# Optimization experiments

Measured on AMD Instinct MI355X. Metric: run time of the kernel, lower is better.

Reference implementation:

```python
import jax, jax.numpy as jnp
import numpy as np

B, S, D, H = 4, 4096, 512, 8


def setup_inputs() -> dict:
    key = jax.random.key(0)
    ks = jax.random.split(key, 9)
    s = 1.0 / np.sqrt(D)
    return {
        "x": jax.random.normal(ks[0], (B, S, D), jnp.float32),
        "Wq": jax.random.normal(ks[1], (D, D), jnp.float32) * s,
        "bq": jax.random.normal(ks[2], (D,), jnp.float32) * 0.02,
        "Wk": jax.random.normal(ks[3], (D, D), jnp.float32) * s,
        "bk": jax.random.normal(ks[4], (D,), jnp.float32) * 0.02,
        "Wv": jax.random.normal(ks[5], (D, D), jnp.float32) * s,
        "bv": jax.random.normal(ks[6], (D,), jnp.float32) * 0.02,
        "Wo": jax.random.normal(ks[7], (H * D, D), jnp.float32) * (1.0 / np.sqrt(H * D)),
        "bo": jax.random.normal(ks[8], (D,), jnp.float32) * 0.02,
        "num_heads": H,
    }


def reference(x, Wq, bq, Wk, bk, Wv, bv, Wo, bo, num_heads):
    # Q/K/V projections (self-attention path; encoder_output=None)
    q = x @ Wq + bq  # [B,S,D]
    k = x @ Wk + bk
    v = x @ Wv + bv
    scale = 1.0 / jnp.sqrt(jnp.asarray(x.shape[-1], x.dtype))
    scores = jnp.einsum("bqd,bkd->bqk", q, k) * scale  # [B,S,S]
    probs = jax.nn.softmax(scores, axis=-1)
    attn = jnp.einsum("bqk,bkd->bqd", probs, v)  # [B,S,D]
    # Original stacks identical heads then torch.cat along dim=-1 -> tile H copies.
    cat = jnp.tile(attn, (1, 1, num_heads))  # [B,S,H*D]
    return cat @ Wo + bo  # [B,S,D]
```

## Files before the change

kernel.cpp:

```cpp
#include <hip/hip_runtime.h>
#include <stdint.h>

#define SCALE 0.04419417382415922f

typedef __bf16 bf16x8 __attribute__((ext_vector_type(8)));
typedef float f32x4 __attribute__((ext_vector_type(4)));
typedef uint16_t u16x8 __attribute__((ext_vector_type(8)));

static __device__ __forceinline__ uint16_t f2bf(float f) {
  union { float f; uint32_t u; } v; v.f = f;
  uint32_t u = v.u;
  return (uint16_t)((u + 0x7FFFu + ((u >> 16) & 1u)) >> 16);
}
static __device__ __forceinline__ float bf2f(uint16_t h) {
  union { uint32_t u; float f; } v; v.u = ((uint32_t)h) << 16;
  return v.f;
}

static __device__ __forceinline__ void gload16(const void* g, void* l) {
  __builtin_amdgcn_global_load_lds(
      (__attribute__((address_space(1))) void*)g,
      (__attribute__((address_space(3))) void*)l, 16, 0, 0);
}

#define P_BAR asm volatile("s_barrier" ::: "memory")
#define P_LGKM do { asm volatile("s_waitcnt lgkmcnt(0)" ::: "memory"); \
                    __builtin_amdgcn_sched_barrier(0); } while (0)


__global__ __launch_bounds__(256)
void convert_x(const float* __restrict__ x, uint16_t* __restrict__ xb) {
  size_t i = ((size_t)blockIdx.x * 256 + threadIdx.x) * 8;
  float4 a = *(const float4*)(x + i);
  float4 b = *(const float4*)(x + i + 4);
  u16x8 o;
  o[0] = f2bf(a.x); o[1] = f2bf(a.y); o[2] = f2bf(a.z); o[3] = f2bf(a.w);
  o[4] = f2bf(b.x); o[5] = f2bf(b.y); o[6] = f2bf(b.z); o[7] = f2bf(b.w);
  *(u16x8*)(xb + i) = o;
}

__global__ __launch_bounds__(256)
void pack_wraw(const float* __restrict__ Wq, const float* __restrict__ Wk,
               uint16_t* __restrict__ oq, uint16_t* __restrict__ ok) {
  size_t i = ((size_t)blockIdx.x * 256 + threadIdx.x) * 8;
  const float* src = blockIdx.y ? Wk : Wq;
  uint16_t* dst = blockIdx.y ? ok : oq;
  const float scl = blockIdx.y ? 1.0f : SCALE;
  float4 a = *(const float4*)(src + i);
  float4 b = *(const float4*)(src + i + 4);
  u16x8 o;
  o[0] = f2bf(a.x * scl); o[1] = f2bf(a.y * scl);
  o[2] = f2bf(a.z * scl); o[3] = f2bf(a.w * scl);
  o[4] = f2bf(b.x * scl); o[5] = f2bf(b.y * scl);
  o[6] = f2bf(b.z * scl); o[7] = f2bf(b.w * scl);
  *(u16x8*)(dst + i) = o;
}

__global__ __launch_bounds__(256)
void pack_wv(const float* __restrict__ Wv, uint16_t* __restrict__ wvT) {
  __shared__ float tile[64][65];
  const int k0 = blockIdx.x * 64, n0 = blockIdx.y * 64;
  const int t = threadIdx.x, r = t >> 2, c0 = (t & 3) * 16;
  #pragma unroll
  for (int j = 0; j < 4; j++) {
    float4 v = *(const float4*)&Wv[(size_t)(k0 + r) * 512 + n0 + c0 + j * 4];
    tile[r][c0 + j * 4 + 0] = v.x; tile[r][c0 + j * 4 + 1] = v.y;
    tile[r][c0 + j * 4 + 2] = v.z; tile[r][c0 + j * 4 + 3] = v.w;
  }
  __syncthreads();
  u16x8 o0, o1;
  #pragma unroll
  for (int e = 0; e < 8; e++) {
    o0[e] = f2bf(tile[c0 + e][r]);
    o1[e] = f2bf(tile[c0 + 8 + e][r]);
  }
  uint16_t* dst = wvT + (size_t)(n0 + r) * 512 + k0 + c0;
  *(u16x8*)dst = o0;
  *(u16x8*)(dst + 8) = o1;
}

__global__ __launch_bounds__(256)
void pack_wo(const float* __restrict__ Wo, uint16_t* __restrict__ woT) {
  __shared__ float tile[64][65];
  const int k0 = blockIdx.x * 64, n0 = blockIdx.y * 64;
  const int t = threadIdx.x, r = t >> 2, c0 = (t & 3) * 16;
  float av[16];
  #pragma unroll
  for (int e = 0; e < 16; e++) av[e] = 0.f;
  for (int h = 0; h < 8; h++) {
    const float* src = &Wo[(size_t)(h * 512 + k0 + r) * 512 + n0 + c0];
    #pragma unroll
    for (int j = 0; j < 4; j++) {
      float4 v = *(const float4*)(src + j * 4);
      av[j * 4 + 0] += v.x; av[j * 4 + 1] += v.y;
      av[j * 4 + 2] += v.z; av[j * 4 + 3] += v.w;
    }
  }
  #pragma unroll
  for (int e = 0; e < 16; e++) tile[r][c0 + e] = av[e];
  __syncthreads();
  u16x8 o0, o1;
  #pragma unroll
  for (int e = 0; e < 8; e++) {
    o0[e] = f2bf(tile[c0 + e][r]);
    o1[e] = f2bf(tile[c0 + 8 + e][r]);
  }
  uint16_t* dst = woT + (size_t)(n0 + r) * 512 + k0 + c0;
  *(u16x8*)dst = o0;
  *(u16x8*)(dst + 8) = o1;
}

__global__ void pack_byv(const float* __restrict__ bv, float* __restrict__ byv) {
  int i = blockIdx.x * 256 + threadIdx.x;
  if (i < 512) byv[i] = 0.f;
  else if (i < 1024) byv[i] = bv[i - 512];
}

__global__ __launch_bounds__(512)
void pack_gc(const float* __restrict__ Wk, const float* __restrict__ bq,
             const float* __restrict__ bk, float* __restrict__ g) {
  __shared__ float red[512];
  const int m = threadIdx.x;
  float s = 0.f;
  for (int d = 0; d < 512; ++d) s += Wk[(size_t)m * 512 + d] * bq[d];
  g[m] = s * SCALE;
  red[m] = bk[m] * bq[m];
  __syncthreads();
  for (int o = 256; o; o >>= 1) {
    if (m < o) red[m] += red[m + o];
    __syncthreads();
  }
  if (m == 0) g[512] = red[0] * SCALE;
}

__global__ __launch_bounds__(256)
void c_vec(const uint16_t* __restrict__ xb, const float* __restrict__ g,
           float* __restrict__ cv) {
  __shared__ float gs[513];
  const int t = threadIdx.x;
  for (int i = t; i < 513; i += 256) gs[i] = g[i];
  __syncthreads();
  const int r = blockIdx.x * 32 + (t >> 3);
  const int j = t & 7;
  const uint16_t* p = xb + (size_t)r * 512 + j * 64;
  float s = 0.f;
  #pragma unroll
  for (int q = 0; q < 8; q++) {
    u16x8 v = *(const u16x8*)(p + q * 8);
    #pragma unroll
    for (int e = 0; e < 8; e++) s += bf2f(v[e]) * gs[j * 64 + q * 8 + e];
  }
  s += __shfl_xor(s, 1); s += __shfl_xor(s, 2); s += __shfl_xor(s, 4);
  if (j == 0) cv[r] = s + gs[512];
}

__global__ __launch_bounds__(256)
void transpose_v(const uint16_t* __restrict__ yv, uint16_t* __restrict__ Vt) {
  __shared__ uint16_t tile[64][72];
  const int s0 = blockIdx.x * 64, d0 = blockIdx.y * 64, b = blockIdx.z;
  const int t = threadIdx.x, r = t >> 2, c0 = (t & 3) * 16;
  const uint16_t* src = yv + ((size_t)(b * 4096 + s0 + r)) * 1024 + 512 + d0 + c0;
  *(u16x8*)&tile[r][c0] = *(const u16x8*)src;
  *(u16x8*)&tile[r][c0 + 8] = *(const u16x8*)(src + 8);
  __syncthreads();
  u16x8 o0, o1;
  #pragma unroll
  for (int e = 0; e < 8; e++) { o0[e] = tile[c0 + e][r]; o1[e] = tile[c0 + 8 + e][r]; }
  uint16_t* dst = Vt + ((size_t)b * 512 + d0 + r) * 4096 + s0 + c0;
  *(u16x8*)dst = o0;
  *(u16x8*)(dst + 8) = o1;
}

template<int BN, int MODE>
static __device__ __forceinline__
void gemm8_body(const uint16_t* __restrict__ A, const uint16_t* __restrict__ Bt,
                const float* __restrict__ bias, void* __restrict__ Cout,
                const float* __restrict__ sums,
                int M, int N, int K, int lda, int ldb, int ldc,
                long long aZ, long long bZ, long long cZ, long long sZ,
                long long biasZ) {
  constexpr int NREP = BN / 64;
  constexpr int NH = NREP / 2;
  constexpr int WN = BN / 4;
  constexpr int BELTS = BN * 64;
  __shared__ uint16_t SH[32768 + 2 * BELTS];

  const int nbn = N / BN;
  const int nwg = (M >> 8) * nbn;
  int id = blockIdx.x;
  id = (id & 7) * (nwg >> 3) + (id >> 3);
  const int bm = id / nbn, bn = id % nbn;
  const long long z = blockIdx.z;
  A += z * aZ; Bt += z * bZ;
  const size_t m0 = (size_t)bm * 256, n0 = (size_t)bn * BN;

  const int t = threadIdx.x;
  const int lane = t & 63, w = t >> 6;
  const int wr = w >> 2, wc = w & 3;
  const int l15 = lane & 15, l4 = lane >> 4, l7 = lane & 7, l3 = lane >> 3;
  const int sw = l7 ^ l3;

  const uint16_t* srcA = A + (m0 + w * 8 + l3) * (size_t)lda + sw * 8;
  const uint16_t* srcB = (BN == 256)
      ? Bt + (n0 + (w >> 1) * 64 + (w & 1) * 16 + l3) * (size_t)ldb + sw * 8
      : Bt + (n0 + (w >> 1) * 32 + (w & 1) * 8 + l3) * (size_t)ldb + sw * 8;

  const int NKT = K >> 6;
  const int NIT = NKT >> 1;

  f32x4 acc[8][NREP];
  #pragma unroll
  for (int i = 0; i < 8; i++)
    #pragma unroll
    for (int j = 0; j < NREP; j++) acc[i][j] = (f32x4)(0.f);

  bf16x8 a[4][2], b0[NH][2], b1[NH][2];

  auto stageA = [&](int tile, int mh) {
    const uint16_t* s = srcA + mh * 64 * (size_t)lda + tile * 64;
    uint16_t* d = SH + (tile & 1) * 16384 + mh * 4096 + w * 512;
    gload16(s, d);
    gload16(s + 128 * (size_t)lda, d + 8192);
  };
  auto stageB = [&](int tile, int nh) {
    if (BN == 256) {
      const uint16_t* s = srcB + nh * 32 * (size_t)ldb + tile * 64;
      uint16_t* d = SH + 32768 + (tile & 1) * BELTS + (w >> 1) * 4096 + nh * 2048 + (w & 1) * 1024;
      gload16(s, d);
      gload16(s + 8 * (size_t)ldb, d + 512);
    } else {
      const uint16_t* s = srcB + nh * 16 * (size_t)ldb + tile * 64;
      uint16_t* d = SH + 32768 + (tile & 1) * BELTS + (w >> 1) * 2048 + nh * 1024 + (w & 1) * 512;
      gload16(s, d);
    }
  };
  auto loadA = [&](int buf, int mh) {
    const uint16_t* base = SH + buf * 16384 + (wr * 128 + mh * 64 + l15) * 64;
    #pragma unroll
    for (int m = 0; m < 4; m++)
      #pragma unroll
      for (int ks = 0; ks < 2; ks++)
        a[m][ks] = *(const bf16x8*)(base + m * 1024 + (((ks * 4 + l4) ^ l7) * 8));
  };
  auto loadB = [&](int buf, int nh, bf16x8 (&bd)[NH][2]) {
    const uint16_t* base = SH + 32768 + buf * BELTS + (wc * WN + nh * (WN / 2) + l15) * 64;
    #pragma unroll
    for (int n = 0; n < NH; n++)
      #pragma unroll
      for (int ks = 0; ks < 2; ks++)
        bd[n][ks] = *(const bf16x8*)(base + n * 1024 + (((ks * 4 + l4) ^ l7) * 8));
  };
  auto quad = [&](int mh, int nq, bf16x8 (&bq)[NH][2]) {
    __builtin_amdgcn_s_setprio(1);
    #pragma unroll
    for (int m = 0; m < 4; m++)
      #pragma unroll
      for (int n = 0; n < NH; n++)
        #pragma unroll
        for (int ks = 0; ks < 2; ks++)
          acc[mh * 4 + m][nq + n] = __builtin_amdgcn_mfma_f32_16x16x32_bf16(
              a[m][ks], bq[n][ks], acc[mh * 4 + m][nq + n], 0, 0, 0);
    __builtin_amdgcn_s_setprio(0);
  };

  stageA(0, 0); stageB(0, 0); stageA(0, 1); stageB(0, 1);
  stageA(1, 0); stageB(1, 0); stageA(1, 1);
  if (BN == 256) asm volatile("s_waitcnt vmcnt(6)" ::: "memory");
  else           asm volatile("s_waitcnt vmcnt(5)" ::: "memory");
  P_BAR;

  for (int k = 0; k < NIT - 1; ++k) {
    const int tt = 2 * k;
    loadA(0, 0); loadB(0, 0, b0); stageB(tt + 1, 1);
    P_BAR; P_LGKM; quad(0, 0, b0); P_BAR;
    loadB(0, 1, b1); stageA(tt + 2, 0);
    P_BAR; P_LGKM; quad(0, NH, b1); P_BAR;
    loadA(0, 1); stageB(tt + 2, 0);
    P_BAR; P_LGKM; quad(1, NH, b1); P_BAR;
    stageA(tt + 2, 1);
    if (BN == 256) asm volatile("s_waitcnt vmcnt(6)" ::: "memory");
    else           asm volatile("s_waitcnt vmcnt(5)" ::: "memory");
    P_BAR; quad(1, 0, b0); P_BAR;
    loadA(1, 0); loadB(1, 0, b0); stageB(tt + 2, 1);
    P_BAR; P_LGKM; quad(0, 0, b0); P_BAR;
    loadB(1, 1, b1); stageA(tt + 3, 0);
    P_BAR; P_LGKM; quad(0, NH, b1); P_BAR;
    loadA(1, 1); stageB(tt + 3, 0);
    P_BAR; P_LGKM; quad(1, NH, b1); P_BAR;
    stageA(tt + 3, 1);
    if (BN == 256) asm volatile("s_waitcnt vmcnt(6)" ::: "memory");
    else           asm volatile("s_waitcnt vmcnt(5)" ::: "memory");
    P_BAR; quad(1, 0, b0); P_BAR;
  }
  loadA(0, 0); loadB(0, 0, b0); stageB(NKT - 1, 1);
  P_BAR; P_LGKM; quad(0, 0, b0); P_BAR;
  loadB(0, 1, b1);
  P_BAR; P_LGKM; quad(0, NH, b1); P_BAR;
  loadA(0, 1);
  P_BAR; P_LGKM; quad(1, NH, b1); P_BAR;
  asm volatile("s_waitcnt vmcnt(0)" ::: "memory");
  P_BAR; quad(1, 0, b0); P_BAR;
  loadA(1, 0); loadB(1, 0, b0);
  P_BAR; P_LGKM; quad(0, 0, b0); P_BAR;
  loadB(1, 1, b1);
  P_BAR; P_LGKM; quad(0, NH, b1); P_BAR;
  loadA(1, 1);
  P_BAR; P_LGKM; quad(1, NH, b1); P_BAR;
  quad(1, 0, b0);

  asm volatile("s_waitcnt vmcnt(0) lgkmcnt(0)" ::: "memory");
  __syncthreads();

  const int g = l4;

  if (MODE == 1) {
    float bvv[NREP];
    #pragma unroll
    for (int ni = 0; ni < NREP; ni++) bvv[ni] = bias[n0 + wc * WN + ni * 16 + l15];
    float* C = (float*)Cout + z * cZ;
    #pragma unroll
    for (int am = 0; am < 8; am++)
      #pragma unroll
      for (int r = 0; r < 4; r++) {
        size_t gr = m0 + wr * 128 + am * 16 + g * 4 + r;
        #pragma unroll
        for (int ni = 0; ni < NREP; ni++)
          C[gr * (size_t)ldc + n0 + wc * WN + ni * 16 + l15] = acc[am][ni][r] + bvv[ni];
      }
    return;
  }

  if (MODE == 2) {
    float cvv[NREP];
    #pragma unroll
    for (int ni = 0; ni < NREP; ni++)
      cvv[ni] = bias[z * biasZ + n0 + wc * WN + ni * 16 + l15];
    float* sm = (float*)Cout;
    (void)sm;
    #pragma unroll
    for (int am = 0; am < 8; am++)
      #pragma unroll
      for (int r = 0; r < 4; r++) {
        float s = 0.f;
        #pragma unroll
        for (int ni = 0; ni < NREP; ni++) {
          float v = __expf(acc[am][ni][r] + cvv[ni]);
          acc[am][ni][r] = v;
          s += v;
        }
        s += __shfl_xor(s, 1); s += __shfl_xor(s, 2);
        s += __shfl_xor(s, 4); s += __shfl_xor(s, 8);
        if (l15 == 0)
          ((float*)sums)[z * sZ + (m0 + wr * 128 + am * 16 + g * 4 + r) * 64 +
                         (n0 >> 6) + wc] = s;
      }
  }

  float bvv[NREP];
  #pragma unroll
  for (int ni = 0; ni < NREP; ni++)
    bvv[ni] = (MODE == 0 && bias) ? bias[n0 + wc * WN + ni * 16 + l15] : 0.f;
  float4 sc[8];
  if (MODE == 3) {
    #pragma unroll
    for (int am = 0; am < 8; am++)
      sc[am] = *(const float4*)&sums[z * sZ + m0 + wr * 128 + am * 16 + g * 4];
  }

  constexpr int STR = BN + 8;
  uint16_t* C16 = (uint16_t*)Cout + z * cZ;
  #pragma unroll
  for (int h = 0; h < 2; ++h) {
    __syncthreads();
    if (wr == h) {
      #pragma unroll
      for (int am = 0; am < 8; am++)
        #pragma unroll
        for (int r = 0; r < 4; r++) {
          const int lr = am * 16 + g * 4 + r;
          #pragma unroll
          for (int ni = 0; ni < NREP; ni++) {
            float v = acc[am][ni][r] + bvv[ni];
            if (MODE == 3) v *= ((const float*)&sc[am])[r];
            SH[lr * STR + wc * WN + ni * 16 + l15] = f2bf(v);
          }
        }
    }
    __syncthreads();
    constexpr int CPT = BN / 32;
    #pragma unroll
    for (int c = 0; c < CPT; ++c) {
      const int idx = t + c * 512;
      const int row = idx / (BN / 8), c8 = idx % (BN / 8);
      *(u16x8*)(C16 + (m0 + h * 128 + row) * (size_t)ldc + n0 + c8 * 8) =
          *(const u16x8*)(SH + row * STR + c8 * 8);
    }
  }
}

__global__ __launch_bounds__(512, 2)
void w2_gemm(const uint16_t* A, const uint16_t* Bt, void* C) {
  gemm8_body<128, 0>(A, Bt, nullptr, C, nullptr, 512, 512, 512, 512, 512, 512,
                     0, 0, 0, 0, 0);
}
__global__ __launch_bounds__(512, 2)
void yv_gemm(const uint16_t* A, const uint16_t* Bt, const float* bias, void* C) {
  gemm8_body<256, 0>(A, Bt, bias, C, nullptr, 16384, 1024, 512, 512, 512, 1024,
                     0, 0, 0, 0, 0);
}
__global__ __launch_bounds__(512, 2)
void scores_gemm(const uint16_t* Y, const uint16_t* X, const float* cvec,
                 void* S, float* sums) {
  gemm8_body<256, 2>(Y, X, cvec, S, sums, 4096, 4096, 512, 1024, 512, 4096,
                     (long long)4096 * 1024, (long long)4096 * 512,
                     (long long)4096 * 4096, (long long)4096 * 64, 4096);
}
__global__ __launch_bounds__(512, 2)
void pv_gemm(const uint16_t* A, const uint16_t* Bt, void* C, const float* inv) {
  gemm8_body<128, 3>(A, Bt, nullptr, C, inv, 4096, 512, 4096, 4096, 4096, 512,
                     (long long)4096 * 4096, (long long)512 * 4096,
                     (long long)4096 * 512, 4096, 0);
}
__global__ __launch_bounds__(512, 2)
void out_gemm(const uint16_t* A, const uint16_t* Bt, const float* bias, void* C) {
  gemm8_body<128, 1>(A, Bt, bias, C, nullptr, 16384, 512, 512, 512, 512, 512,
                     0, 0, 0, 0, 0);
}

__global__ __launch_bounds__(256)
void reduce_sums(const float* __restrict__ P, float* __restrict__ inv, int rows) {
  int r = blockIdx.x * 256 + threadIdx.x;
  if (r >= rows) return;
  const float4* p4 = (const float4*)(P + (size_t)r * 64);
  float s = 0.f;
  #pragma unroll
  for (int i = 0; i < 16; ++i) { float4 v = p4[i]; s += (v.x + v.y) + (v.z + v.w); }
  inv[r] = 1.f / s;
}


extern "C" void kernel_launch(void* const* d_in, const int* in_sizes, int n_in,
                              void* d_out, int out_size, void* d_ws, size_t ws_size,
                              hipStream_t stream) {
  const float* x   = (const float*)d_in[0];
  const float* Wq  = (const float*)d_in[1];
  const float* bq  = (const float*)d_in[2];
  const float* Wk  = (const float*)d_in[3];
  const float* bk  = (const float*)d_in[4];
  const float* Wv  = (const float*)d_in[5];
  const float* bvp = (const float*)d_in[6];
  const float* Wo  = (const float*)d_in[7];
  const float* bo  = (const float*)d_in[8];
  float* out = (float*)d_out;

  char* ws = (char*)d_ws;
  const size_t MB = (size_t)1 << 20;
  uint16_t* xb   = (uint16_t*)(ws);
  uint16_t* yv   = (uint16_t*)(ws + 16 * MB);
  uint16_t* Vt   = (uint16_t*)(ws + 48 * MB);
  uint16_t* attn = (uint16_t*)(ws + 64 * MB);
  uint16_t* wqs  = (uint16_t*)(ws + 80 * MB);
  uint16_t* wkr  = (uint16_t*)(ws + 80 * MB + 512 * 1024);
  uint16_t* w2T  = (uint16_t*)(ws + 81 * MB);
  uint16_t* wvT  = (uint16_t*)(ws + 81 * MB + 512 * 1024);
  uint16_t* woT  = (uint16_t*)(ws + 82 * MB);
  float*    byv  = (float*)   (ws + 82 * MB + 512 * 1024);
  float*    g    = (float*)   (ws + 83 * MB);
  float*    sums = (float*)   (ws + 84 * MB);
  float*    invs = (float*)   (ws + 88 * MB);
  float*    cv   = (float*)   (ws + 89 * MB);
  uint16_t* Sbuf = (uint16_t*)(ws + 96 * MB);

  const int nz = (ws_size >= 225 * MB) ? 4 : 2;

  convert_x<<<dim3(4096), dim3(256), 0, stream>>>(x, xb);
  pack_wraw<<<dim3(128, 2), dim3(256), 0, stream>>>(Wq, Wk, wqs, wkr);
  pack_wv<<<dim3(8, 8), dim3(256), 0, stream>>>(Wv, wvT);
  pack_wo<<<dim3(8, 8), dim3(256), 0, stream>>>(Wo, woT);
  pack_byv<<<dim3(4), dim3(256), 0, stream>>>(bvp, byv);
  pack_gc<<<dim3(1), dim3(512), 0, stream>>>(Wk, bq, bk, g);

  w2_gemm<<<dim3(8, 1, 1), dim3(512), 0, stream>>>(wkr, wqs, w2T);

  yv_gemm<<<dim3(256, 1, 1), dim3(512), 0, stream>>>(xb, w2T, byv, yv);

  transpose_v<<<dim3(64, 8, 4), dim3(256), 0, stream>>>(yv, Vt);
  c_vec<<<dim3(512), dim3(256), 0, stream>>>(xb, g, cv);

  for (int p = 0; p < 4 / nz; ++p) {
    const uint16_t* Yp = yv + (size_t)p * nz * 4096 * 1024;
    const uint16_t* Xp = xb + (size_t)p * nz * 4096 * 512;
    const float* cp = cv + (size_t)p * nz * 4096;
    float* sp = sums + (size_t)p * nz * 4096 * 64;
    float* ip = invs + (size_t)p * nz * 4096;
    scores_gemm<<<dim3(256, 1, nz), dim3(512), 0, stream>>>(Yp, Xp, cp, Sbuf, sp);
    reduce_sums<<<dim3(nz * 4096 / 256), dim3(256), 0, stream>>>(sp, ip, nz * 4096);
    pv_gemm<<<dim3(64, 1, nz), dim3(512), 0, stream>>>(
        Sbuf, Vt + (size_t)p * nz * 512 * 4096, attn + (size_t)p * nz * 4096 * 512, ip);
  }

  out_gemm<<<dim3(256, 1, 1), dim3(512), 0, stream>>>(attn, woT, bo, out);
}
```

Measured before the change: 304.7 us.

## Fold Wo into V projection and fuse output GEMM into PV epilogue

Precomputes Wv·Wo_sum as a single 512x512 weight (and bv·Wo_sum as the bias) so the yv GEMM produces V already projected through the output matrix. The PV GEMM then applies the softmax normalisation and bo in its epilogue and writes fp32 output directly, removing the separate out_gemm pass and the bf16 attn buffer. The bias-vector setup kernels are split into parallel GEMVs. The composed weight is rounded to bf16 once more, which adds some precision risk.

```diff
diff --git a/kernel.cpp b/kernel.cpp
--- a/kernel.cpp
+++ b/kernel.cpp
@@ -41,11 +41,14 @@
 
 __global__ __launch_bounds__(256)
 void pack_wraw(const float* __restrict__ Wq, const float* __restrict__ Wk,
-               uint16_t* __restrict__ oq, uint16_t* __restrict__ ok) {
+               const float* __restrict__ Wv,
+               uint16_t* __restrict__ oq, uint16_t* __restrict__ ok,
+               uint16_t* __restrict__ ov) {
   size_t i = ((size_t)blockIdx.x * 256 + threadIdx.x) * 8;
-  const float* src = blockIdx.y ? Wk : Wq;
-  uint16_t* dst = blockIdx.y ? ok : oq;
-  const float scl = blockIdx.y ? 1.0f : SCALE;
+  const int m = blockIdx.y;
+  const float* src = (m == 0) ? Wq : ((m == 1) ? Wk : Wv);
+  uint16_t* dst = (m == 0) ? oq : ((m == 1) ? ok : ov);
+  const float scl = (m == 0) ? SCALE : 1.0f;
   float4 a = *(const float4*)(src + i);
   float4 b = *(const float4*)(src + i + 4);
   u16x8 o;
@@ -57,29 +60,6 @@
 }
 
 __global__ __launch_bounds__(256)
-void pack_wv(const float* __restrict__ Wv, uint16_t* __restrict__ wvT) {
-  __shared__ float tile[64][65];
-  const int k0 = blockIdx.x * 64, n0 = blockIdx.y * 64;
-  const int t = threadIdx.x, r = t >> 2, c0 = (t & 3) * 16;
-  #pragma unroll
-  for (int j = 0; j < 4; j++) {
-    float4 v = *(const float4*)&Wv[(size_t)(k0 + r) * 512 + n0 + c0 + j * 4];
-    tile[r][c0 + j * 4 + 0] = v.x; tile[r][c0 + j * 4 + 1] = v.y;
-    tile[r][c0 + j * 4 + 2] = v.z; tile[r][c0 + j * 4 + 3] = v.w;
-  }
-  __syncthreads();
-  u16x8 o0, o1;
-  #pragma unroll
-  for (int e = 0; e < 8; e++) {
-    o0[e] = f2bf(tile[c0 + e][r]);
-    o1[e] = f2bf(tile[c0 + 8 + e][r]);
-  }
-  uint16_t* dst = wvT + (size_t)(n0 + r) * 512 + k0 + c0;
-  *(u16x8*)dst = o0;
-  *(u16x8*)(dst + 8) = o1;
-}
-
-__global__ __launch_bounds__(256)
 void pack_wo(const float* __restrict__ Wo, uint16_t* __restrict__ woT) {
   __shared__ float tile[64][65];
   const int k0 = blockIdx.x * 64, n0 = blockIdx.y * 64;
@@ -110,27 +90,57 @@
   *(u16x8*)(dst + 8) = o1;
 }
 
-__global__ void pack_byv(const float* __restrict__ bv, float* __restrict__ byv) {
-  int i = blockIdx.x * 256 + threadIdx.x;
-  if (i < 512) byv[i] = 0.f;
-  else if (i < 1024) byv[i] = bv[i - 512];
-}
-
-__global__ __launch_bounds__(512)
-void pack_gc(const float* __restrict__ Wk, const float* __restrict__ bq,
-             const float* __restrict__ bk, float* __restrict__ g) {
-  __shared__ float red[512];
-  const int m = threadIdx.x;
+__global__ __launch_bounds__(256)
+void gemv_g(const float* __restrict__ Wk, const float* __restrict__ bq,
+            float* __restrict__ g) {
+  __shared__ float vs[512];
+  const int t = threadIdx.x;
+  vs[t] = bq[t]; vs[t + 256] = bq[t + 256];
+  __syncthreads();
+  const int r = blockIdx.x * 32 + (t >> 3), j = t & 7;
+  const float4* p = (const float4*)(Wk + (size_t)r * 512 + j * 64);
   float s = 0.f;
-  for (int d = 0; d < 512; ++d) s += Wk[(size_t)m * 512 + d] * bq[d];
-  g[m] = s * SCALE;
-  red[m] = bk[m] * bq[m];
-  __syncthreads();
-  for (int o = 256; o; o >>= 1) {
-    if (m < o) red[m] += red[m + o];
-    __syncthreads();
-  }
-  if (m == 0) g[512] = red[0] * SCALE;
+  #pragma unroll
+  for (int q = 0; q < 16; q++) {
+    float4 v = p[q];
+    const float* b = &vs[j * 64 + q * 4];
+    s += v.x * b[0] + v.y * b[1] + v.z * b[2] + v.w * b[3];
+  }
+  s += __shfl_xor(s, 1); s += __shfl_xor(s, 2); s += __shfl_xor(s, 4);
+  if (j == 0) g[r] = s * SCALE;
+}
+
+__global__ __launch_bounds__(256)
+void kappa_calc(const float* __restrict__ bq, const float* __restrict__ bk,
+                float* __restrict__ g) {
+  const int t = threadIdx.x;
+  float s = bq[t] * bk[t] + bq[t + 256] * bk[t + 256];
+  #pragma unroll
+  for (int o = 32; o; o >>= 1) s += __shfl_xor(s, o);
+  __shared__ float rr[4];
+  if ((t & 63) == 0) rr[t >> 6] = s;
+  __syncthreads();
+  if (t == 0) g[512] = (rr[0] + rr[1] + rr[2] + rr[3]) * SCALE;
+}
+
+__global__ __launch_bounds__(256)
+void gemv_bvo(const uint16_t* __restrict__ woT, const float* __restrict__ bv,
+              float* __restrict__ out) {
+  __shared__ float vs[512];
+  const int t = threadIdx.x;
+  vs[t] = bv[t]; vs[t + 256] = bv[t + 256];
+  __syncthreads();
+  const int r = blockIdx.x * 32 + (t >> 3), j = t & 7;
+  const u16x8* p = (const u16x8*)(woT + (size_t)r * 512 + j * 64);
+  float s = 0.f;
+  #pragma unroll
+  for (int q = 0; q < 8; q++) {
+    u16x8 v = p[q];
+    #pragma unroll
+    for (int e = 0; e < 8; e++) s += bf2f(v[e]) * vs[j * 64 + q * 8 + e];
+  }
+  s += __shfl_xor(s, 1); s += __shfl_xor(s, 2); s += __shfl_xor(s, 4);
+  if (j == 0) out[r] = s;
 }
 
 __global__ __launch_bounds__(256)
@@ -313,10 +323,16 @@
 
   const int g = l4;
 
-  if (MODE == 1) {
+  if (MODE == 1 || MODE == 4) {
     float bvv[NREP];
     #pragma unroll
     for (int ni = 0; ni < NREP; ni++) bvv[ni] = bias[n0 + wc * WN + ni * 16 + l15];
+    float4 sc[8];
+    if (MODE == 4) {
+      #pragma unroll
+      for (int am = 0; am < 8; am++)
+        sc[am] = *(const float4*)&sums[z * sZ + m0 + wr * 128 + am * 16 + g * 4];
+    }
     float* C = (float*)Cout + z * cZ;
     #pragma unroll
     for (int am = 0; am < 8; am++)
@@ -324,8 +340,11 @@
       for (int r = 0; r < 4; r++) {
         size_t gr = m0 + wr * 128 + am * 16 + g * 4 + r;
         #pragma unroll
-        for (int ni = 0; ni < NREP; ni++)
-          C[gr * (size_t)ldc + n0 + wc * WN + ni * 16 + l15] = acc[am][ni][r] + bvv[ni];
+        for (int ni = 0; ni < NREP; ni++) {
+          float v = acc[am][ni][r];
+          if (MODE == 4) v *= ((const float*)&sc[am])[r];
+          C[gr * (size_t)ldc + n0 + wc * WN + ni * 16 + l15] = v + bvv[ni];
+        }
       }
     return;
   }
@@ -335,8 +354,6 @@
     #pragma unroll
     for (int ni = 0; ni < NREP; ni++)
       cvv[ni] = bias[z * biasZ + n0 + wc * WN + ni * 16 + l15];
-    float* sm = (float*)Cout;
-    (void)sm;
     #pragma unroll
     for (int am = 0; am < 8; am++)
       #pragma unroll
@@ -360,12 +377,6 @@
   #pragma unroll
   for (int ni = 0; ni < NREP; ni++)
     bvv[ni] = (MODE == 0 && bias) ? bias[n0 + wc * WN + ni * 16 + l15] : 0.f;
-  float4 sc[8];
-  if (MODE == 3) {
-    #pragma unroll
-    for (int am = 0; am < 8; am++)
-      sc[am] = *(const float4*)&sums[z * sZ + m0 + wr * 128 + am * 16 + g * 4];
-  }
 
   constexpr int STR = BN + 8;
   uint16_t* C16 = (uint16_t*)Cout + z * cZ;
@@ -381,7 +392,6 @@
           #pragma unroll
           for (int ni = 0; ni < NREP; ni++) {
             float v = acc[am][ni][r] + bvv[ni];
-            if (MODE == 3) v *= ((const float*)&sc[am])[r];
             SH[lr * STR + wc * WN + ni * 16 + l15] = f2bf(v);
           }
         }
@@ -400,6 +410,11 @@
 
 __global__ __launch_bounds__(512, 2)
 void w2_gemm(const uint16_t* A, const uint16_t* Bt, void* C) {
+  gemm8_body<128, 0>(A, Bt, nullptr, C, nullptr, 512, 512, 512, 512, 512, 512,
+                     0, 0, 0, 0, 0);
+}
+__global__ __launch_bounds__(512, 2)
+void wvo_gemm(const uint16_t* A, const uint16_t* Bt, void* C) {
   gemm8_body<128, 0>(A, Bt, nullptr, C, nullptr, 512, 512, 512, 512, 512, 512,
                      0, 0, 0, 0, 0);
 }
@@ -416,15 +431,11 @@
                      (long long)4096 * 4096, (long long)4096 * 64, 4096);
 }
 __global__ __launch_bounds__(512, 2)
-void pv_gemm(const uint16_t* A, const uint16_t* Bt, void* C, const float* inv) {
-  gemm8_body<128, 3>(A, Bt, nullptr, C, inv, 4096, 512, 4096, 4096, 4096, 512,
+void pvo_gemm(const uint16_t* A, const uint16_t* Bt, const float* bias,
+              void* C, const float* inv) {
+  gemm8_body<128, 4>(A, Bt, bias, C, inv, 4096, 512, 4096, 4096, 4096, 512,
                      (long long)4096 * 4096, (long long)512 * 4096,
                      (long long)4096 * 512, 4096, 0);
-}
-__global__ __launch_bounds__(512, 2)
-void out_gemm(const uint16_t* A, const uint16_t* Bt, const float* bias, void* C) {
-  gemm8_body<128, 1>(A, Bt, bias, C, nullptr, 16384, 512, 512, 512, 512, 512,
-                     0, 0, 0, 0, 0);
 }
 
 __global__ __launch_bounds__(256)
@@ -458,46 +469,59 @@
   uint16_t* xb   = (uint16_t*)(ws);
   uint16_t* yv   = (uint16_t*)(ws + 16 * MB);
   uint16_t* Vt   = (uint16_t*)(ws + 48 * MB);
-  uint16_t* attn = (uint16_t*)(ws + 64 * MB);
   uint16_t* wqs  = (uint16_t*)(ws + 80 * MB);
   uint16_t* wkr  = (uint16_t*)(ws + 80 * MB + 512 * 1024);
-  uint16_t* w2T  = (uint16_t*)(ws + 81 * MB);
-  uint16_t* wvT  = (uint16_t*)(ws + 81 * MB + 512 * 1024);
+  uint16_t* yvW  = (uint16_t*)(ws + 81 * MB);
+  uint16_t* w2T  = yvW;
+  uint16_t* wvoT = yvW + (size_t)512 * 512;
   uint16_t* woT  = (uint16_t*)(ws + 82 * MB);
-  float*    byv  = (float*)   (ws + 82 * MB + 512 * 1024);
-  float*    g    = (float*)   (ws + 83 * MB);
+  uint16_t* wvr  = (uint16_t*)(ws + 82 * MB + 512 * 1024);
+  float*    byv  = (float*)   (ws + 83 * MB);
+  float*    g    = (float*)   (ws + 83 * MB + 8 * 1024);
   float*    sums = (float*)   (ws + 84 * MB);
   float*    invs = (float*)   (ws + 88 * MB);
   float*    cv   = (float*)   (ws + 89 * MB);
   uint16_t* Sbuf = (uint16_t*)(ws + 96 * MB);
 
-  const int nz = (ws_size >= 225 * MB) ? 4 : 2;
+  const int big = (ws_size >= 225 * MB);
 
   convert_x<<<dim3(4096), dim3(256), 0, stream>>>(x, xb);
-  pack_wraw<<<dim3(128, 2), dim3(256), 0, stream>>>(Wq, Wk, wqs, wkr);
-  pack_wv<<<dim3(8, 8), dim3(256), 0, stream>>>(Wv, wvT);
+  pack_wraw<<<dim3(128, 3), dim3(256), 0, stream>>>(Wq, Wk, Wv, wqs, wkr, wvr);
   pack_wo<<<dim3(8, 8), dim3(256), 0, stream>>>(Wo, woT);
-  pack_byv<<<dim3(4), dim3(256), 0, stream>>>(bvp, byv);
-  pack_gc<<<dim3(1), dim3(512), 0, stream>>>(Wk, bq, bk, g);
+  gemv_g<<<dim3(16), dim3(256), 0, stream>>>(Wk, bq, g);
+  kappa_calc<<<dim3(1), dim3(256), 0, stream>>>(bq, bk, g);
+  hipMemsetAsync(byv, 0, 512 * sizeof(float), stream);
+  gemv_bvo<<<dim3(16), dim3(256), 0, stream>>>(woT, bvp, byv + 512);
 
   w2_gemm<<<dim3(8, 1, 1), dim3(512), 0, stream>>>(wkr, wqs, w2T);
-
-  yv_gemm<<<dim3(256, 1, 1), dim3(512), 0, stream>>>(xb, w2T, byv, yv);
+  wvo_gemm<<<dim3(8, 1, 1), dim3(512), 0, stream>>>(woT, wvr, wvoT);
+
+  yv_gemm<<<dim3(256, 1, 1), dim3(512), 0, stream>>>(xb, yvW, byv, yv);
 
   transpose_v<<<dim3(64, 8, 4), dim3(256), 0, stream>>>(yv, Vt);
   c_vec<<<dim3(512), dim3(256), 0, stream>>>(xb, g, cv);
 
-  for (int p = 0; p < 4 / nz; ++p) {
-    const uint16_t* Yp = yv + (size_t)p * nz * 4096 * 1024;
-    const uint16_t* Xp = xb + (size_t)p * nz * 4096 * 512;
-    const float* cp = cv + (size_t)p * nz * 4096;
-    float* sp = sums + (size_t)p * nz * 4096 * 64;
-    float* ip = invs + (size_t)p * nz * 4096;
-    scores_gemm<<<dim3(256, 1, nz), dim3(512), 0, stream>>>(Yp, Xp, cp, Sbuf, sp);
-    reduce_sums<<<dim3(nz * 4096 / 256), dim3(256), 0, stream>>>(sp, ip, nz * 4096);
-    pv_gemm<<<dim3(64, 1, nz), dim3(512), 0, stream>>>(
-        Sbuf, Vt + (size_t)p * nz * 512 * 4096, attn + (size_t)p * nz * 4096 * 512, ip);
-  }
-
-  out_gemm<<<dim3(256, 1, 1), dim3(512), 0, stream>>>(attn, woT, bo, out);
-}
+  if (big) {
+    for (int p = 0; p < 2; ++p) {
+      scores_gemm<<<dim3(256, 1, 2), dim3(512), 0, stream>>>(
+          yv + (size_t)p * 2 * 4096 * 1024, xb + (size_t)p * 2 * 4096 * 512,
+          cv + (size_t)p * 2 * 4096, Sbuf + (size_t)p * 2 * 4096 * 4096,
+          sums + (size_t)p * 2 * 4096 * 64);
+      reduce_sums<<<dim3(2 * 4096 / 256), dim3(256), 0, stream>>>(
+          sums + (size_t)p * 2 * 4096 * 64, invs + (size_t)p * 2 * 4096, 2 * 4096);
+    }
+    pvo_gemm<<<dim3(64, 1, 4), dim3(512), 0, stream>>>(Sbuf, Vt, bo, out, invs);
+  } else {
+    for (int p = 0; p < 2; ++p) {
+      scores_gemm<<<dim3(256, 1, 2), dim3(512), 0, stream>>>(
+          yv + (size_t)p * 2 * 4096 * 1024, xb + (size_t)p * 2 * 4096 * 512,
+          cv + (size_t)p * 2 * 4096, Sbuf,
+          sums + (size_t)p * 2 * 4096 * 64);
+      reduce_sums<<<dim3(2 * 4096 / 256), dim3(256), 0, stream>>>(
+          sums + (size_t)p * 2 * 4096 * 64, invs + (size_t)p * 2 * 4096, 2 * 4096);
+      pvo_gemm<<<dim3(64, 1, 2), dim3(512), 0, stream>>>(
+          Sbuf, Vt + (size_t)p * 2 * 512 * 4096, bo,
+          out + (size_t)p * 2 * 4096 * 512, invs + (size_t)p * 2 * 4096);
+    }
+  }
+}
```

After: 282.5 us. 7.3% less time.
